# Optimization experiments

Measured on AMD Instinct MI355X. Metric: run time of the kernel, lower is better.

## Reference

```python
import jax, jax.numpy as jnp
import numpy as np

# Intrinsics (KITTI odometry full resolution)
H, W = 376, 1241
FX, FY, CX, CY = 718.856, 718.856, 607.1928, 185.2157
B = 128

# pixels_grid = np.c_[np.meshgrid(arange(W), arange(H))] -> (2, H, W), [0]=x, [1]=y
_gx, _gy = np.meshgrid(np.arange(W, dtype=np.float32), np.arange(H, dtype=np.float32))
GRID_X = jnp.asarray(_gx)  # (H, W)
GRID_Y = jnp.asarray(_gy)  # (H, W)
# intrinsics.forward: pixel -> normalized camera coords; append ones -> (3, H, W)
PIX_NORM = jnp.stack([(GRID_X - CX) / FX, (GRID_Y - CY) / FY, jnp.ones((H, W), jnp.float32)], axis=0)


def _euler_to_R(r):
    """Euler angles (rx, ry, rz) -> rotation matrix R = Rz @ Ry @ Rx."""
    cx, sx = jnp.cos(r[0]), jnp.sin(r[0])
    cy, sy = jnp.cos(r[1]), jnp.sin(r[1])
    cz, sz = jnp.cos(r[2]), jnp.sin(r[2])
    Rx = jnp.array([[1.0, 0.0, 0.0], [0.0, cx, -sx], [0.0, sx, cx]])
    Ry = jnp.array([[cy, 0.0, sy], [0.0, 1.0, 0.0], [-sy, 0.0, cy]])
    Rz = jnp.array([[cz, -sz, 0.0], [sz, cz, 0.0], [0.0, 0.0, 1.0]])
    return Rz @ Ry @ Rx


def setup_inputs() -> dict:
    key = jax.random.key(0)
    k1, _ = jax.random.split(key)
    rotations = jax.random.normal(k1, (B, 3), dtype=jnp.float32) * 0.05  # small camera rotations (rad)
    depth = jnp.ones((H, W), dtype=jnp.float32)
    translation = jnp.zeros((3,), dtype=jnp.float32)
    return {"rotations": rotations, "depth": depth, "translation": translation}


def reference(rotations, depth, translation):
    Rs = jax.vmap(_euler_to_R)(rotations)                      # (B, 3, 3)
    points1 = depth[None] * PIX_NORM                           # (3, H, W)
    p = points1.reshape(3, -1) - translation[:, None]          # (3, H*W)
    # points2 = R.T @ p, batched
    points2 = jnp.einsum('bji,jn->bin', Rs, p)                 # (B, 3, H*W)
    points2 = points2.reshape(B, 3, H, W)
    z = points2[:, 2]
    # intrinsics.backward: normalized -> pixel coords
    x_pix = points2[:, 0] / z * FX + CX                        # (B, H, W)
    y_pix = points2[:, 1] / z * FY + CY
    flow_x = (x_pix - GRID_X) / W                              # gt_flow[...,0] /= width
    flow_y = (y_pix - GRID_Y) / H                              # gt_flow[...,1] /= height
    return jnp.stack([flow_x, flow_y], axis=-1).astype(jnp.float32)  # (B, H, W, 2)
```

## Files before the change

kernel.cpp:

```cpp
#include <hip/hip_runtime.h>

constexpr int   H  = 376, W = 1241, B = 128;
constexpr int   HW = H * W;
constexpr int   NPAIR = HW / 2;
constexpr float FXc = 718.856f, FYc = 718.856f;
constexpr float CXc = 607.1928f, CYc = 185.2157f;

typedef float  vfloat4 __attribute__((ext_vector_type(4)));
typedef float  vfloat2 __attribute__((ext_vector_type(2)));

__global__ __launch_bounds__(256) void flow_main_kernel(
        const float* __restrict__ rot,
        const float* __restrict__ trans,
        const float* __restrict__ depth,
        float* __restrict__ out) {
    const int b = blockIdx.y;

    __shared__ float4 Ms[3];
    if (threadIdx.x == 0) {
        float rx = rot[b * 3 + 0], ry = rot[b * 3 + 1], rz = rot[b * 3 + 2];
        float cx = cosf(rx), sx = sinf(rx);
        float cy = cosf(ry), sy = sinf(ry);
        float cz = cosf(rz), sz = sinf(rz);
        float m00 = cz * cy,                m01 = sz * cy,                m02 = -sy;
        float m10 = cz * sy * sx - sz * cx, m11 = sz * sy * sx + cz * cx, m12 = cy * sx;
        float m20 = cz * sy * cx + sz * sx, m21 = sz * sy * cx - cz * sx, m22 = cy * cx;
        float t0 = trans[0], t1 = trans[1], t2 = trans[2];
        Ms[0] = make_float4(m00, m01, m02, m00 * t0 + m01 * t1 + m02 * t2);
        Ms[1] = make_float4(m10, m11, m12, m10 * t0 + m11 * t1 + m12 * t2);
        Ms[2] = make_float4(m20, m21, m22, m20 * t0 + m21 * t1 + m22 * t2);
    }
    __syncthreads();

    const int u = blockIdx.x * 256 + threadIdx.x;
    if (u >= NPAIR) return;
    const int n0 = u * 2;

    const float4 r0 = Ms[0];
    const float4 r1 = Ms[1];
    const float4 r2 = Ms[2];

    const vfloat2 d2 = *reinterpret_cast<const vfloat2*>(depth + n0);

    int y0 = n0 / W;
    int x0 = n0 - y0 * W;
    int x1 = x0 + 1, y1 = y0;
    if (x1 == W) { x1 = 0; y1 += 1; }

    float xs[2] = { (float)x0, (float)x1 };
    float ys[2] = { (float)y0, (float)y1 };
    float ds[2] = { d2.x, d2.y };
    float fo[4];

#pragma unroll
    for (int i = 0; i < 2; ++i) {
        float px = (xs[i] - CXc) * (1.0f / FXc);
        float py = (ys[i] - CYc) * (1.0f / FYc);
        float s0 = fmaf(r0.x, px, fmaf(r0.y, py, r0.z));
        float s1 = fmaf(r1.x, px, fmaf(r1.y, py, r1.z));
        float s2 = fmaf(r2.x, px, fmaf(r2.y, py, r2.z));
        float d  = ds[i];
        float q0 = fmaf(d, s0, -r0.w);
        float q1 = fmaf(d, s1, -r1.w);
        float q2 = fmaf(d, s2, -r2.w);
        float inv = __builtin_amdgcn_rcpf(q2);
        fo[2 * i + 0] = fmaf(q0 * inv, FXc, CXc - xs[i]) * (1.0f / (float)W);
        fo[2 * i + 1] = fmaf(q1 * inv, FYc, CYc - ys[i]) * (1.0f / (float)H);
    }

    vfloat4 o;
    o.x = fo[0]; o.y = fo[1]; o.z = fo[2]; o.w = fo[3];
    const size_t off = ((size_t)b * HW + n0) * 2;
    __builtin_nontemporal_store(o, reinterpret_cast<vfloat4*>(out + off));
}

extern "C" void kernel_launch(void* const* d_in, const int* in_sizes, int n_in,
                              void* d_out, int out_size, void* d_ws, size_t ws_size,
                              hipStream_t stream) {
    const float* rotations   = (const float*)d_in[0];
    const float* depth       = (const float*)d_in[1];
    const float* translation = (const float*)d_in[2];
    float*       out         = (float*)d_out;

    dim3 grid((NPAIR + 255) / 256, B);
    flow_main_kernel<<<grid, 256, 0, stream>>>(rotations, translation, depth, out);
}
```

Baseline: 87.45 us.

## Switch to persistent grid-stride loop with depth prefetch

```diff
diff --git a/kernel.cpp b/kernel.cpp
--- a/kernel.cpp
+++ b/kernel.cpp
@@ -3,13 +3,15 @@
 constexpr int   H  = 376, W = 1241, B = 128;
 constexpr int   HW = H * W;
 constexpr int   NPAIR = HW / 2;
+constexpr int   GX = 16;
+constexpr int   STRIDE = GX * 256;
 constexpr float FXc = 718.856f, FYc = 718.856f;
 constexpr float CXc = 607.1928f, CYc = 185.2157f;
 
 typedef float  vfloat4 __attribute__((ext_vector_type(4)));
 typedef float  vfloat2 __attribute__((ext_vector_type(2)));
 
-__global__ __launch_bounds__(256) void flow_main_kernel(
+__global__ __launch_bounds__(256, 8) void flow_main_kernel(
         const float* __restrict__ rot,
         const float* __restrict__ trans,
         const float* __restrict__ depth,
@@ -32,46 +34,55 @@
     }
     __syncthreads();
 
-    const int u = blockIdx.x * 256 + threadIdx.x;
-    if (u >= NPAIR) return;
-    const int n0 = u * 2;
-
     const float4 r0 = Ms[0];
     const float4 r1 = Ms[1];
     const float4 r2 = Ms[2];
 
-    const vfloat2 d2 = *reinterpret_cast<const vfloat2*>(depth + n0);
+    float* __restrict__ outb = out + (size_t)b * HW * 2;
 
-    int y0 = n0 / W;
-    int x0 = n0 - y0 * W;
-    int x1 = x0 + 1, y1 = y0;
-    if (x1 == W) { x1 = 0; y1 += 1; }
+    int u = blockIdx.x * 256 + threadIdx.x;
+    vfloat2 d = *reinterpret_cast<const vfloat2*>(depth + 2 * u);
 
-    float xs[2] = { (float)x0, (float)x1 };
-    float ys[2] = { (float)y0, (float)y1 };
-    float ds[2] = { d2.x, d2.y };
-    float fo[4];
+    while (true) {
+        const int  un   = u + STRIDE;
+        const bool more = (un < NPAIR);
+        vfloat2 dn;
+        if (more) dn = *reinterpret_cast<const vfloat2*>(depth + 2 * un);
+
+        const int n0 = u * 2;
+        int y0 = n0 / W;
+        int x0 = n0 - y0 * W;
+        int x1 = x0 + 1, y1 = y0;
+        if (x1 == W) { x1 = 0; y1 += 1; }
+
+        float xs[2] = { (float)x0, (float)x1 };
+        float ys[2] = { (float)y0, (float)y1 };
+        float ds[2] = { d.x, d.y };
+        float fo[4];
 
 #pragma unroll
-    for (int i = 0; i < 2; ++i) {
-        float px = (xs[i] - CXc) * (1.0f / FXc);
-        float py = (ys[i] - CYc) * (1.0f / FYc);
-        float s0 = fmaf(r0.x, px, fmaf(r0.y, py, r0.z));
-        float s1 = fmaf(r1.x, px, fmaf(r1.y, py, r1.z));
-        float s2 = fmaf(r2.x, px, fmaf(r2.y, py, r2.z));
-        float d  = ds[i];
-        float q0 = fmaf(d, s0, -r0.w);
-        float q1 = fmaf(d, s1, -r1.w);
-        float q2 = fmaf(d, s2, -r2.w);
-        float inv = __builtin_amdgcn_rcpf(q2);
-        fo[2 * i + 0] = fmaf(q0 * inv, FXc, CXc - xs[i]) * (1.0f / (float)W);
-        fo[2 * i + 1] = fmaf(q1 * inv, FYc, CYc - ys[i]) * (1.0f / (float)H);
+        for (int i = 0; i < 2; ++i) {
+            float px = (xs[i] - CXc) * (1.0f / FXc);
+            float py = (ys[i] - CYc) * (1.0f / FYc);
+            float s0 = fmaf(r0.x, px, fmaf(r0.y, py, r0.z));
+            float s1 = fmaf(r1.x, px, fmaf(r1.y, py, r1.z));
+            float s2 = fmaf(r2.x, px, fmaf(r2.y, py, r2.z));
+            float dd = ds[i];
+            float q0 = fmaf(dd, s0, -r0.w);
+            float q1 = fmaf(dd, s1, -r1.w);
+            float q2 = fmaf(dd, s2, -r2.w);
+            float inv = __builtin_amdgcn_rcpf(q2);
+            fo[2 * i + 0] = fmaf(q0 * inv, FXc, CXc - xs[i]) * (1.0f / (float)W);
+            fo[2 * i + 1] = fmaf(q1 * inv, FYc, CYc - ys[i]) * (1.0f / (float)H);
+        }
+
+        vfloat4 o;
+        o.x = fo[0]; o.y = fo[1]; o.z = fo[2]; o.w = fo[3];
+        __builtin_nontemporal_store(o, reinterpret_cast<vfloat4*>(outb + 4 * (size_t)u));
+
+        if (!more) break;
+        u = un; d = dn;
     }
-
-    vfloat4 o;
-    o.x = fo[0]; o.y = fo[1]; o.z = fo[2]; o.w = fo[3];
-    const size_t off = ((size_t)b * HW + n0) * 2;
-    __builtin_nontemporal_store(o, reinterpret_cast<vfloat4*>(out + off));
 }
 
 extern "C" void kernel_launch(void* const* d_in, const int* in_sizes, int n_in,
@@ -82,6 +93,6 @@
     const float* translation = (const float*)d_in[2];
     float*       out         = (float*)d_out;
 
-    dim3 grid((NPAIR + 255) / 256, B);
+    dim3 grid(GX, B);
     flow_main_kernel<<<grid, 256, 0, stream>>>(rotations, translation, depth, out);
 }
```

Measured after the change: 103.1 us. 17.9% more time.
